# Performance work log

Hardware: AMD Instinct MI355X
Metric: run time of the kernel (lower is better)

The kernel has to match this reference:

```python
import jax, jax.numpy as jnp
import numpy as np

K = 3          # conv kernel size
STRIDE = 1     # conv stride (SAME padding)
ITERS = 3      # DR routing iterations
EPS = 1e-9     # squash epsilon


def squash(s, axis):
    # v = ||s||^2 / (1 + ||s||^2) * s / ||s||   (DR squash)
    sq = jnp.sum(s * s, axis=axis, keepdims=True)
    return (sq / (1.0 + sq)) * s * jax.lax.rsqrt(sq + EPS)


def setup_inputs() -> dict:
    key = jax.random.key(0)
    k1, k2, k3 = jax.random.split(key, 3)
    b, h, w, iCaps, iPose = 8, 12, 12, 32, 16
    oCaps, oPose = 32, 16
    x = jax.random.normal(k1, (b, h, w, iCaps, iPose), dtype=jnp.float32)
    # Wa: [kk*iCaps, oCaps, iPose, oPose] (leading 1 of the TF weight is dropped)
    fan = K * K * iCaps * iPose
    W = jax.random.normal(k2, (K * K * iCaps, oCaps, iPose, oPose), dtype=jnp.float32) * np.float32(np.sqrt(2.0 / fan))
    # biases: [oCaps, oPose] (TF shape [1,1,oCaps,oPose,1], broadcastable)
    biases = jax.random.normal(k3, (oCaps, oPose), dtype=jnp.float32) * 0.05
    return {"x": x, "W": W, "biases": biases}


def _kernel_tile(x2d):
    # im2col for SAME padding, stride 1.  x2d: (b, h, w, C) -> (b, h, w, k*k, C)
    b, h, w, C = x2d.shape
    pad = K // 2
    xp = jnp.pad(x2d, ((0, 0), (pad, pad), (pad, pad), (0, 0)))
    patches = jnp.stack(
        [xp[:, i:i + h, j:j + w, :] for i in range(K) for j in range(K)], axis=3
    )
    return patches  # (b, h, w, k*k, C)


def reference(x, W, biases):
    b, h, w, iCaps, iPose = x.shape
    iC = K * K * iCaps
    oC, oP = biases.shape

    # 1. kernel_tile: gather k*k neighborhoods
    patches = _kernel_tile(x.reshape(b, h, w, iCaps * iPose))      # (b,h,w,kk,iCaps*iPose)
    u = patches.reshape(b * h * w, iC, iPose)                       # (bx, iC, iPose)

    # 2. transform_view (vector capsules): votes[n,i,c,:] = u[n,i,:] @ W[i,c,:,:]
    votes = jnp.einsum('nip,icpq->nicq', u, W)                      # (bx, iC, oC, oP)

    # 3. DR routing
    bx = votes.shape[0]
    logits = jnp.zeros((bx, iC, oC), dtype=votes.dtype)
    v = None
    for ii in range(ITERS):
        c = jax.nn.softmax(logits, axis=2)                          # coupling coeffs over oCaps
        s = jnp.einsum('nic,nicq->ncq', c, votes) + biases          # (bx, oC, oP)
        v = squash(s, axis=2)
        if ii < ITERS - 1:
            logits = logits + jnp.einsum('nicq,ncq->nic', votes, v)  # agreement

    return v.reshape(b, h, w, oC, oP)
```

## Files before the change

kernel.cpp:

```cpp
#include <hip/hip_runtime.h>
#include <stdint.h>

typedef unsigned short ushort_t;

#define KK3 3
#define IC 32
#define IP 16
#define OC 32
#define OP 16
#define NI 288
#define HH 12
#define WWW 12
#define NTOT 1152
#define CQ 512
#define EPSQ 1e-9f
#define RWAVES 4
#define RSTEPS 36

__device__ __forceinline__ float bf_lo(unsigned u) { return __uint_as_float(u << 16); }
__device__ __forceinline__ float bf_hi(unsigned u) { return __uint_as_float(u & 0xffff0000u); }
__device__ __forceinline__ ushort_t f2bf(float f) {
    unsigned u = __float_as_uint(f);
    return (ushort_t)((u + 0x7fffu + ((u >> 16) & 1u)) >> 16);
}

__global__ __launch_bounds__(128) void votes_kernel(
    const float* __restrict__ x, const float* __restrict__ Wg,
    ushort_t* __restrict__ votes, int nStart, int nCount)
{
    __shared__ float u_lds[64][IP];

    const int i = blockIdx.x;
    const int tileBase = blockIdx.y * 64;
    const int nC = min(64, nCount - tileBase);
    const int t = threadIdx.x;
    const int c = t >> 2;
    const int qq = t & 3;

    const int ky = i / (KK3 * IC);
    const int kx = (i / IC) % KK3;
    const int ic = i % IC;

    {
        const int nl = t >> 1;
        const int ph = (t & 1) * 8;
        if (nl < nC) {
            const int n = nStart + tileBase + nl;
            const int b = n / (HH * WWW);
            const int rem = n % (HH * WWW);
            const int y = rem / WWW;
            const int xx = rem % WWW;
            const int sy = y + ky - 1;
            const int sx = xx + kx - 1;
            float4 v0 = make_float4(0.f, 0.f, 0.f, 0.f), v1 = v0;
            if (sy >= 0 && sy < HH && sx >= 0 && sx < WWW) {
                const float* src = x + ((((size_t)b * HH + sy) * WWW + sx) * IC + ic) * IP + ph;
                v0 = *(const float4*)(src);
                v1 = *(const float4*)(src + 4);
            }
            *(float4*)&u_lds[nl][ph] = v0;
            *(float4*)&u_lds[nl][ph + 4] = v1;
        }
    }

    float4 w[IP];
    {
        const float* wb = Wg + ((size_t)i * OC + c) * (IP * OP) + qq * 4;
#pragma unroll
        for (int p = 0; p < IP; ++p) w[p] = *(const float4*)(wb + p * OP);
    }
    __syncthreads();

    ushort_t* vb = votes + ((size_t)tileBase * NI + i) * CQ + c * OP + qq * 4;
    for (int nl = 0; nl < nC; ++nl) {
        const float4 u0 = *(const float4*)&u_lds[nl][0];
        const float4 u1 = *(const float4*)&u_lds[nl][4];
        const float4 u2 = *(const float4*)&u_lds[nl][8];
        const float4 u3 = *(const float4*)&u_lds[nl][12];
        float a0 = 0.f, a1 = 0.f, a2 = 0.f, a3 = 0.f;
#define ACC(uf, pp)                                         \
        a0 = fmaf(uf, w[pp].x, a0); a1 = fmaf(uf, w[pp].y, a1); \
        a2 = fmaf(uf, w[pp].z, a2); a3 = fmaf(uf, w[pp].w, a3);
        ACC(u0.x, 0)  ACC(u0.y, 1)  ACC(u0.z, 2)  ACC(u0.w, 3)
        ACC(u1.x, 4)  ACC(u1.y, 5)  ACC(u1.z, 6)  ACC(u1.w, 7)
        ACC(u2.x, 8)  ACC(u2.y, 9)  ACC(u2.z, 10) ACC(u2.w, 11)
        ACC(u3.x, 12) ACC(u3.y, 13) ACC(u3.z, 14) ACC(u3.w, 15)
#undef ACC
        ushort4 st;
        st.x = f2bf(a0); st.y = f2bf(a1); st.z = f2bf(a2); st.w = f2bf(a3);
        *(ushort4*)vb = st;
        vb += (size_t)NI * CQ;
    }
}

#define UNPACK16(A, B)                                                     \
    const float f0 = bf_lo(A.x), f1 = bf_hi(A.x), f2 = bf_lo(A.y),         \
                f3 = bf_hi(A.y), f4 = bf_lo(A.z), f5 = bf_hi(A.z),         \
                f6 = bf_lo(A.w), f7 = bf_hi(A.w), f8 = bf_lo(B.x),         \
                f9 = bf_hi(B.x), f10 = bf_lo(B.y), f11 = bf_hi(B.y),       \
                f12 = bf_lo(B.z), f13 = bf_hi(B.z), f14 = bf_lo(B.w),      \
                f15 = bf_hi(B.w);

__global__ __launch_bounds__(256) void route_kernel(
    const ushort_t* __restrict__ votes, const float* __restrict__ bias,
    float* __restrict__ out, int nStart)
{
    __shared__ float lg_lds[NI * OC];
    __shared__ float sPart[RWAVES][CQ];
    __shared__ float s_sh[CQ];
    __shared__ float v_sh[CQ];
    __shared__ float fac_sh[OC];

    const int bn = blockIdx.x;
    const int t = threadIdx.x;
    const int wv = t >> 6;
    const int l = t & 63;
    const int isub = l >> 5;
    const int c = l & 31;
    const int iBase = 2 * wv + isub;

    const ushort_t* pbase = votes + (size_t)bn * NI * CQ + (size_t)iBase * CQ + c * OP;
    const size_t stepB = (size_t)8 * CQ;

    float sa[16];

#pragma unroll
    for (int q = 0; q < 16; ++q) sa[q] = 0.f;
    {
        uint4 A = ((const uint4*)pbase)[0];
        uint4 B = ((const uint4*)pbase)[1];
#pragma unroll 4
        for (int r = 0; r < RSTEPS; ++r) {
            uint4 An, Bn;
            if (r + 1 < RSTEPS) {
                const uint4* pn = (const uint4*)(pbase + (size_t)(r + 1) * stepB);
                An = pn[0]; Bn = pn[1];
            }
            UNPACK16(A, B)
            sa[0] += f0;  sa[1] += f1;  sa[2] += f2;  sa[3] += f3;
            sa[4] += f4;  sa[5] += f5;  sa[6] += f6;  sa[7] += f7;
            sa[8] += f8;  sa[9] += f9;  sa[10] += f10; sa[11] += f11;
            sa[12] += f12; sa[13] += f13; sa[14] += f14; sa[15] += f15;
            A = An; B = Bn;
        }
    }
#pragma unroll
    for (int q = 0; q < 16; ++q) sa[q] += __shfl_xor(sa[q], 32);
    if (isub == 0) {
#pragma unroll
        for (int k = 0; k < 4; ++k)
            *(float4*)&sPart[wv][c * 16 + 4 * k] = make_float4(sa[4*k], sa[4*k+1], sa[4*k+2], sa[4*k+3]);
    }

    float vr[16];
#pragma unroll
    for (int it = 0; it <= 2; ++it) {
        __syncthreads();
#pragma unroll
        for (int rep = 0; rep < 2; ++rep) {
            const int k = t + rep * 256;
            float s = (sPart[0][k] + sPart[1][k]) + (sPart[2][k] + sPart[3][k]);
            s_sh[k] = fmaf(s, (it == 0) ? (1.0f / OC) : 1.0f, bias[k]);
        }
        __syncthreads();
        if (t < OC) {
            float sq = 0.f;
#pragma unroll
            for (int q = 0; q < OP; ++q) { const float s = s_sh[t * OP + q]; sq = fmaf(s, s, sq); }
            fac_sh[t] = (sq / (1.0f + sq)) * rsqrtf(sq + EPSQ);
        }
        __syncthreads();
#pragma unroll
        for (int rep = 0; rep < 2; ++rep) {
            const int k = t + rep * 256;
            v_sh[k] = s_sh[k] * fac_sh[k >> 4];
        }
        __syncthreads();
        if (it == 2) break;

#pragma unroll
        for (int k = 0; k < 4; ++k) {
            const float4 v4 = *(const float4*)&v_sh[c * 16 + 4 * k];
            vr[4*k] = v4.x; vr[4*k+1] = v4.y; vr[4*k+2] = v4.z; vr[4*k+3] = v4.w;
        }
#pragma unroll
        for (int q = 0; q < 16; ++q) sa[q] = 0.f;
        uint4 A = ((const uint4*)pbase)[0];
        uint4 B = ((const uint4*)pbase)[1];
#pragma unroll 4
        for (int r = 0; r < RSTEPS; ++r) {
            uint4 An, Bn;
            if (r + 1 < RSTEPS) {
                const uint4* pn = (const uint4*)(pbase + (size_t)(r + 1) * stepB);
                An = pn[0]; Bn = pn[1];
            }
            UNPACK16(A, B)
            float a = f0 * vr[0];
            a = fmaf(f1, vr[1], a);   a = fmaf(f2, vr[2], a);   a = fmaf(f3, vr[3], a);
            a = fmaf(f4, vr[4], a);   a = fmaf(f5, vr[5], a);   a = fmaf(f6, vr[6], a);
            a = fmaf(f7, vr[7], a);   a = fmaf(f8, vr[8], a);   a = fmaf(f9, vr[9], a);
            a = fmaf(f10, vr[10], a); a = fmaf(f11, vr[11], a); a = fmaf(f12, vr[12], a);
            a = fmaf(f13, vr[13], a); a = fmaf(f14, vr[14], a); a = fmaf(f15, vr[15], a);
            const int li = (iBase + 8 * r) * OC + c;
            if (it == 0) lg_lds[li] = a;
            else          a += lg_lds[li];
            const float e = __expf(a);
            float es = e;
            es += __shfl_xor(es, 1);
            es += __shfl_xor(es, 2);
            es += __shfl_xor(es, 4);
            es += __shfl_xor(es, 8);
            es += __shfl_xor(es, 16);
            const float coup = __fdividef(e, es);
            sa[0] = fmaf(coup, f0, sa[0]);   sa[1] = fmaf(coup, f1, sa[1]);
            sa[2] = fmaf(coup, f2, sa[2]);   sa[3] = fmaf(coup, f3, sa[3]);
            sa[4] = fmaf(coup, f4, sa[4]);   sa[5] = fmaf(coup, f5, sa[5]);
            sa[6] = fmaf(coup, f6, sa[6]);   sa[7] = fmaf(coup, f7, sa[7]);
            sa[8] = fmaf(coup, f8, sa[8]);   sa[9] = fmaf(coup, f9, sa[9]);
            sa[10] = fmaf(coup, f10, sa[10]); sa[11] = fmaf(coup, f11, sa[11]);
            sa[12] = fmaf(coup, f12, sa[12]); sa[13] = fmaf(coup, f13, sa[13]);
            sa[14] = fmaf(coup, f14, sa[14]); sa[15] = fmaf(coup, f15, sa[15]);
            A = An; B = Bn;
        }
#pragma unroll
        for (int q = 0; q < 16; ++q) sa[q] += __shfl_xor(sa[q], 32);
        if (isub == 0) {
#pragma unroll
            for (int k = 0; k < 4; ++k)
                *(float4*)&sPart[wv][c * 16 + 4 * k] = make_float4(sa[4*k], sa[4*k+1], sa[4*k+2], sa[4*k+3]);
        }
    }

#pragma unroll
    for (int rep = 0; rep < 2; ++rep) {
        const int k = t + rep * 256;
        out[(size_t)(nStart + bn) * CQ + k] = v_sh[k];
    }
}

extern "C" void kernel_launch(void* const* d_in, const int* in_sizes, int n_in,
                              void* d_out, int out_size, void* d_ws, size_t ws_size,
                              hipStream_t stream)
{
    const float* x = (const float*)d_in[0];
    const float* Wg = (const float*)d_in[1];
    const float* bias = (const float*)d_in[2];
    float* out = (float*)d_out;
    ushort_t* votes = (ushort_t*)d_ws;

    const size_t perN = (size_t)NI * CQ * sizeof(ushort_t);
    size_t fit = ws_size / perN;
    int chunk = (fit >= 576) ? 576 : (int)fit;
    if (chunk < 1) chunk = 1;

    for (int start = 0; start < NTOT; start += chunk) {
        const int cnt = (NTOT - start < chunk) ? (NTOT - start) : chunk;
        dim3 gA(NI, (cnt + 63) / 64);
        hipLaunchKernelGGL(votes_kernel, gA, dim3(128), 0, stream, x, Wg, votes, start, cnt);
        hipLaunchKernelGGL(route_kernel, dim3(cnt), dim3(256), 0, stream, votes, bias, out, start);
    }
}
```

Baseline: 259.9 us.

## Compute first routing iteration as MFMA GEMM instead of summing votes

Because the first routing iteration uses uniform coupling, s0 equals the sum over input capsules of votes, which is an im2col GEMM of x against W. The change packs W to bf16 in an MFMA layout and computes s0 for all pixels with a 16x16x32 bf16 MFMA kernel, so route_kernel skips the first full pass over the votes buffer. Chunk size drops from 576 to 288 to make room for the packed weights and the s0 buffer in the workspace. This adds two extra launches and more votes/route launch pairs, and it converts x to bf16 for the GEMM, which may change rounding.

```diff
diff --git a/kernel.cpp b/kernel.cpp
--- a/kernel.cpp
+++ b/kernel.cpp
@@ -16,12 +16,86 @@
 #define EPSQ 1e-9f
 #define RWAVES 4
 #define RSTEPS 36
+#define NIP 144
+
+typedef __attribute__((ext_vector_type(8))) short bf16x8;
+typedef __attribute__((ext_vector_type(4))) float f32x4;
 
 __device__ __forceinline__ float bf_lo(unsigned u) { return __uint_as_float(u << 16); }
 __device__ __forceinline__ float bf_hi(unsigned u) { return __uint_as_float(u & 0xffff0000u); }
 __device__ __forceinline__ ushort_t f2bf(float f) {
     unsigned u = __float_as_uint(f);
     return (ushort_t)((u + 0x7fffu + ((u >> 16) & 1u)) >> 16);
+}
+
+__global__ __launch_bounds__(64) void pack_kernel(
+    const float* __restrict__ W, ushort_t* __restrict__ Wp)
+{
+    const int blk = blockIdx.x;
+    const int ip = blk >> 5;
+    const int c = blk & 31;
+    const int l = threadIdx.x;
+    const int i = ip * 2 + ((l >> 5) & 1);
+    const int p0 = ((l >> 4) & 1) * 8;
+    const int q = l & 15;
+    const float* src = W + (((size_t)(i * 32 + c) * 16 + p0) * 16 + q);
+    union { ushort_t s[8]; uint4 u4; } o;
+#pragma unroll
+    for (int j = 0; j < 8; ++j) o.s[j] = f2bf(src[(size_t)j * 16]);
+    *(uint4*)(Wp + ((size_t)blk * 64 + l) * 8) = o.u4;
+}
+
+__global__ __launch_bounds__(64) void s0_gemm_kernel(
+    const float* __restrict__ x, const ushort_t* __restrict__ Wp,
+    float* __restrict__ s0_pre)
+{
+    const int l = threadIdx.x;
+    const int pxt = blockIdx.x;
+    const int cb = blockIdx.y * 8;
+    const int px = pxt * 16 + (l & 15);
+    const int b = px / (HH * WWW);
+    const int rem = px % (HH * WWW);
+    const int y = rem / WWW;
+    const int xx = rem % WWW;
+    const int ioff = (l >> 5) & 1;
+    const int p0 = ((l >> 4) & 1) * 8;
+
+    f32x4 acc[8];
+#pragma unroll
+    for (int ct = 0; ct < 8; ++ct) acc[ct] = (f32x4){0.f, 0.f, 0.f, 0.f};
+
+    for (int ip = 0; ip < NIP; ++ip) {
+        const int i = ip * 2 + ioff;
+        const int ky = i / (KK3 * IC);
+        const int kx = (i / IC) % KK3;
+        const int ic = i & (IC - 1);
+        const int sy = y + ky - 1;
+        const int sx = xx + kx - 1;
+        union { ushort_t s[8]; bf16x8 v; } ua;
+        if (sy >= 0 && sy < HH && sx >= 0 && sx < WWW) {
+            const float* s = x + ((((size_t)b * HH + sy) * WWW + sx) * IC + ic) * IP + p0;
+            const float4 v0 = *(const float4*)s;
+            const float4 v1 = *(const float4*)(s + 4);
+            ua.s[0] = f2bf(v0.x); ua.s[1] = f2bf(v0.y); ua.s[2] = f2bf(v0.z); ua.s[3] = f2bf(v0.w);
+            ua.s[4] = f2bf(v1.x); ua.s[5] = f2bf(v1.y); ua.s[6] = f2bf(v1.z); ua.s[7] = f2bf(v1.w);
+        } else {
+#pragma unroll
+            for (int j = 0; j < 8; ++j) ua.s[j] = 0;
+        }
+#pragma unroll
+        for (int ct = 0; ct < 8; ++ct) {
+            const bf16x8 bv = *(const bf16x8*)(Wp + (((size_t)ip * 32 + (cb + ct)) * 64 + l) * 8);
+            acc[ct] = __builtin_amdgcn_mfma_f32_16x16x32_bf16(ua.v, bv, acc[ct], 0, 0, 0);
+        }
+    }
+
+    const int prow = pxt * 16 + (l >> 4) * 4;
+    const int q = l & 15;
+#pragma unroll
+    for (int ct = 0; ct < 8; ++ct)
+#pragma unroll
+        for (int r = 0; r < 4; ++r)
+            s0_pre[(size_t)(prow + r) * CQ + (size_t)(cb + ct) * 16 + q] = acc[ct][r];
 }
 
 __global__ __launch_bounds__(128) void votes_kernel(
@@ -102,8 +176,8 @@
                 f15 = bf_hi(B.w);
 
 __global__ __launch_bounds__(256) void route_kernel(
-    const ushort_t* __restrict__ votes, const float* __restrict__ bias,
-    float* __restrict__ out, int nStart)
+    const ushort_t* __restrict__ votes, const float* __restrict__ s0_pre,
+    const float* __restrict__ bias, float* __restrict__ out, int nStart)
 {
     __shared__ float lg_lds[NI * OC];
     __shared__ float sPart[RWAVES][CQ];
@@ -122,62 +196,31 @@
     const ushort_t* pbase = votes + (size_t)bn * NI * CQ + (size_t)iBase * CQ + c * OP;
     const size_t stepB = (size_t)8 * CQ;
 
+#pragma unroll
+    for (int rep = 0; rep < 2; ++rep) {
+        const int k = t + rep * 256;
+        s_sh[k] = fmaf(s0_pre[(size_t)(nStart + bn) * CQ + k], 1.0f / OC, bias[k]);
+    }
+    __syncthreads();
+    if (t < OC) {
+        float sq = 0.f;
+#pragma unroll
+        for (int q = 0; q < OP; ++q) { const float s = s_sh[t * OP + q]; sq = fmaf(s, s, sq); }
+        fac_sh[t] = (sq / (1.0f + sq)) * rsqrtf(sq + EPSQ);
+    }
+    __syncthreads();
+#pragma unroll
+    for (int rep = 0; rep < 2; ++rep) {
+        const int k = t + rep * 256;
+        v_sh[k] = s_sh[k] * fac_sh[k >> 4];
+    }
+    __syncthreads();
+
     float sa[16];
-
-#pragma unroll
-    for (int q = 0; q < 16; ++q) sa[q] = 0.f;
-    {
-        uint4 A = ((const uint4*)pbase)[0];
-        uint4 B = ((const uint4*)pbase)[1];
-#pragma unroll 4
-        for (int r = 0; r < RSTEPS; ++r) {
-            uint4 An, Bn;
-            if (r + 1 < RSTEPS) {
-                const uint4* pn = (const uint4*)(pbase + (size_t)(r + 1) * stepB);
-                An = pn[0]; Bn = pn[1];
-            }
-            UNPACK16(A, B)
-            sa[0] += f0;  sa[1] += f1;  sa[2] += f2;  sa[3] += f3;
-            sa[4] += f4;  sa[5] += f5;  sa[6] += f6;  sa[7] += f7;
-            sa[8] += f8;  sa[9] += f9;  sa[10] += f10; sa[11] += f11;
-            sa[12] += f12; sa[13] += f13; sa[14] += f14; sa[15] += f15;
-            A = An; B = Bn;
-        }
-    }
-#pragma unroll
-    for (int q = 0; q < 16; ++q) sa[q] += __shfl_xor(sa[q], 32);
-    if (isub == 0) {
-#pragma unroll
-        for (int k = 0; k < 4; ++k)
-            *(float4*)&sPart[wv][c * 16 + 4 * k] = make_float4(sa[4*k], sa[4*k+1], sa[4*k+2], sa[4*k+3]);
-    }
-
     float vr[16];
-#pragma unroll
-    for (int it = 0; it <= 2; ++it) {
-        __syncthreads();
-#pragma unroll
-        for (int rep = 0; rep < 2; ++rep) {
-            const int k = t + rep * 256;
-            float s = (sPart[0][k] + sPart[1][k]) + (sPart[2][k] + sPart[3][k]);
-            s_sh[k] = fmaf(s, (it == 0) ? (1.0f / OC) : 1.0f, bias[k]);
-        }
-        __syncthreads();
-        if (t < OC) {
-            float sq = 0.f;
-#pragma unroll
-            for (int q = 0; q < OP; ++q) { const float s = s_sh[t * OP + q]; sq = fmaf(s, s, sq); }
-            fac_sh[t] = (sq / (1.0f + sq)) * rsqrtf(sq + EPSQ);
-        }
-        __syncthreads();
-#pragma unroll
-        for (int rep = 0; rep < 2; ++rep) {
-            const int k = t + rep * 256;
-            v_sh[k] = s_sh[k] * fac_sh[k >> 4];
-        }
-        __syncthreads();
-        if (it == 2) break;
-
+
+#pragma unroll
+    for (int it = 0; it < 2; ++it) {
 #pragma unroll
         for (int k = 0; k < 4; ++k) {
             const float4 v4 = *(const float4*)&v_sh[c * 16 + 4 * k];
@@ -229,6 +272,27 @@
             for (int k = 0; k < 4; ++k)
                 *(float4*)&sPart[wv][c * 16 + 4 * k] = make_float4(sa[4*k], sa[4*k+1], sa[4*k+2], sa[4*k+3]);
         }
+        __syncthreads();
+#pragma unroll
+        for (int rep = 0; rep < 2; ++rep) {
+            const int k = t + rep * 256;
+            float s = (sPart[0][k] + sPart[1][k]) + (sPart[2][k] + sPart[3][k]);
+            s_sh[k] = s + bias[k];
+        }
+        __syncthreads();
+        if (t < OC) {
+            float sq = 0.f;
+#pragma unroll
+            for (int q = 0; q < OP; ++q) { const float s = s_sh[t * OP + q]; sq = fmaf(s, s, sq); }
+            fac_sh[t] = (sq / (1.0f + sq)) * rsqrtf(sq + EPSQ);
+        }
+        __syncthreads();
+#pragma unroll
+        for (int rep = 0; rep < 2; ++rep) {
+            const int k = t + rep * 256;
+            v_sh[k] = s_sh[k] * fac_sh[k >> 4];
+        }
+        __syncthreads();
     }
 
 #pragma unroll
@@ -246,17 +310,31 @@
     const float* Wg = (const float*)d_in[1];
     const float* bias = (const float*)d_in[2];
     float* out = (float*)d_out;
+
+    const size_t perN = (size_t)NI * CQ * sizeof(ushort_t);
+    const size_t packBytes = (size_t)NIP * 32 * 64 * 8 * 2;
+    const size_t s0Bytes = (size_t)NTOT * CQ * sizeof(float);
+
+    int chunk = 288;
+    if (ws_size < (size_t)chunk * perN + packBytes + s0Bytes) {
+        size_t avail = (ws_size > packBytes + s0Bytes) ? ws_size - packBytes - s0Bytes : 0;
+        chunk = (int)(avail / perN);
+        if (chunk < 1) chunk = 1;
+    }
+    const size_t packOff = (size_t)chunk * perN;
+    const size_t s0Off = packOff + packBytes;
+
     ushort_t* votes = (ushort_t*)d_ws;
-
-    const size_t perN = (size_t)NI * CQ * sizeof(ushort_t);
-    size_t fit = ws_size / perN;
-    int chunk = (fit >= 576) ? 576 : (int)fit;
-    if (chunk < 1) chunk = 1;
+    ushort_t* Wp = (ushort_t*)((char*)d_ws + packOff);
+    float* s0_pre = (float*)((char*)d_ws + s0Off);
+
+    hipLaunchKernelGGL(pack_kernel, dim3(NIP * 32), dim3(64), 0, stream, Wg, Wp);
+    hipLaunchKernelGGL(s0_gemm_kernel, dim3(NTOT / 16, 4), dim3(64), 0, stream, x, Wp, s0_pre);
 
     for (int start = 0; start < NTOT; start += chunk) {
         const int cnt = (NTOT - start < chunk) ? (NTOT - start) : chunk;
         dim3 gA(NI, (cnt + 63) / 64);
         hipLaunchKernelGGL(votes_kernel, gA, dim3(128), 0, stream, x, Wg, votes, start, cnt);
-        hipLaunchKernelGGL(route_kernel, dim3(cnt), dim3(256), 0, stream, votes, bias, out, start);
-    }
-}
+        hipLaunchKernelGGL(route_kernel, dim3(cnt), dim3(256), 0, stream, votes, s0_pre, bias, out, start);
+    }
+}
```

Result: slower. 351.8 us (+35.4%).
